# Kernel tuning notes

Hardware: AMD Instinct MI355X
Metric: run time of the kernel (lower is better)

## Reference

```python
import jax, jax.numpy as jnp
import numpy as np

CAPACITY = 8_388_608  # 2**23, power of two -> leftmost_leaf == capacity
N_UPDATES = 1_048_576  # 2**20


def setup_inputs() -> dict:
    key = jax.random.key(0)
    k1, k2, k3 = jax.random.split(key, 3)
    # Existing tree buffer; values[1] is root, values[CAPACITY:2*CAPACITY] are leaves.
    tree_values = jax.random.uniform(k1, (2 * CAPACITY,), dtype=jnp.float32)
    # Distinct leaf indices in [0, CAPACITY): torch scatter-assign with duplicate
    # indices is nondeterministic, so the meaningful case is distinct indices.
    indices = jax.random.permutation(k2, CAPACITY)[:N_UPDATES].astype(jnp.int32)
    values = jax.random.uniform(k3, (N_UPDATES,), dtype=jnp.float32)
    return {"tree_values": tree_values, "indices": indices, "values": values}


def reference(tree_values, indices, values):
    """SegmentTree.__setitem__ with op=add: set leaves, propagate sums to root.

    Returns the updated (2*capacity,) tree buffer.
    """
    capacity = tree_values.shape[0] // 2  # static python int
    depth = int(capacity).bit_length() - 1  # log2(capacity) levels to the root
    # _index_to_leaf: with power-of-two capacity, leaf = idx + capacity (no wrap).
    leaf = indices.astype(jnp.int32) + capacity
    tree = tree_values.at[leaf].set(values)
    idx = leaf
    # Original does torch.unique(idx//2) per level purely as an optimization;
    # duplicate parents recompute the identical value, so plain scatter-set of
    # op(left_child, right_child) is the same math and jit-friendly.
    for _ in range(depth):
        idx = idx // 2
        parent = tree[2 * idx] + tree[2 * idx + 1]
        tree = tree.at[idx].set(parent)
    return tree
```

## Files before the change

kernel.cpp:

```cpp
#include <hip/hip_runtime.h>


typedef unsigned int uint;
typedef unsigned char uchar;

#define NB_COARSE 256
#define CCAP 4608
#define FCAP 512
#define NPB 4096

__global__ void clear_kernel(uint* __restrict__ gcursor) {
    gcursor[threadIdx.x] = threadIdx.x * CCAP;
}

__global__ __launch_bounds__(256)
void coarse_bin_kernel(const int* __restrict__ idx,
                       const float* __restrict__ val,
                       uint* __restrict__ gcursor,
                       uint2* __restrict__ coarse) {
    __shared__ uint hist[NB_COARSE], rbase[NB_COARSE], cur[NB_COARSE];
    const int tid = threadIdx.x;
    hist[tid] = 0u;
    __syncthreads();

    const int i0 = blockIdx.x * NPB;
    uint j[16]; float v[16];
    #pragma unroll
    for (int e = 0; e < 16; ++e) {
        int i = i0 + e * 256 + tid;
        j[e] = (uint)idx[i];
        v[e] = val[i];
        atomicAdd(&hist[j[e] >> 15], 1u);
    }
    __syncthreads();
    rbase[tid] = hist[tid] ? atomicAdd(&gcursor[tid], hist[tid]) : 0u;
    cur[tid] = 0u;
    __syncthreads();
    #pragma unroll
    for (int e = 0; e < 16; ++e) {
        uint cb = j[e] >> 15;
        uint pos = rbase[cb] + atomicAdd(&cur[cb], 1u);
        if (pos < (cb + 1u) * CCAP)
            coarse[pos] = make_uint2(j[e], __float_as_uint(v[e]));
    }
}

__global__ __launch_bounds__(256)
void fine_bin_kernel(const uint* __restrict__ gcursor,
                     const uint2* __restrict__ coarse,
                     uint* __restrict__ fcnt,
                     uint2* __restrict__ fbins) {
    __shared__ uint fcur[16];
    const int b = blockIdx.x, tid = threadIdx.x;
    if (tid < 16) fcur[tid] = 0u;
    __syncthreads();
    uint nb = gcursor[b] - (uint)b * CCAP;
    if (nb > CCAP) nb = CCAP;
    const uint2* my = coarse + (size_t)b * CCAP;
    for (uint k = tid; k < nb; k += 256u) {
        uint2 e = my[k];
        uint fb = (e.x >> 11) & 15u;
        uint r = atomicAdd(&fcur[fb], 1u);
        if (r < FCAP)
            fbins[(((size_t)b * 16u + fb) << 9) + r] = e;
    }
    __syncthreads();
    if (tid < 16) {
        uint c = fcur[tid];
        fcnt[b * 16 + tid] = c > FCAP ? FCAP : c;
    }
}

__global__ __launch_bounds__(256)
void merge_kernel(const float* __restrict__ tree,
                  const uint* __restrict__ fcnt,
                  const uint2* __restrict__ fbins,
                  uchar* __restrict__ l11flag,
                  float* __restrict__ out, int C) {
    __shared__ float slv[2048];
    __shared__ uchar sfl[2048];
    __shared__ float sv[256];
    __shared__ uint  sd[256];

    const int b   = blockIdx.x;
    const int tid = threadIdx.x;

    ((uint2*)sfl)[tid] = make_uint2(0u, 0u);
    __syncthreads();
    uint c = fcnt[b];
    const uint2* mybin = fbins + ((size_t)b << 9);
    for (uint k = tid; k < c; k += 256u) {
        uint2 e = mybin[k];
        uint off = e.x & 2047u;
        slv[off] = __uint_as_float(e.y);
        sfl[off] = 1;
    }
    __syncthreads();

    const int leaf0  = tid * 8;
    const int gleaf0 = b * 2048 + leaf0;

    uint2 fw = *(const uint2*)&sfl[leaf0];
    float4 la = *(const float4*)&slv[leaf0];
    float4 lb = *(const float4*)&slv[leaf0 + 4];
    float4 ta = *(const float4*)(tree + C + gleaf0);
    float4 tb = *(const float4*)(tree + C + gleaf0 + 4);

    float l0 = (fw.x & 0x000000FFu) ? la.x : ta.x;
    float l1 = (fw.x & 0x0000FF00u) ? la.y : ta.y;
    float l2 = (fw.x & 0x00FF0000u) ? la.z : ta.z;
    float l3 = (fw.x & 0xFF000000u) ? la.w : ta.w;
    float l4 = (fw.y & 0x000000FFu) ? lb.x : tb.x;
    float l5 = (fw.y & 0x0000FF00u) ? lb.y : tb.y;
    float l6 = (fw.y & 0x00FF0000u) ? lb.z : tb.z;
    float l7 = (fw.y & 0xFF000000u) ? lb.w : tb.w;

    *(float4*)(out + C + gleaf0)     = make_float4(l0, l1, l2, l3);
    *(float4*)(out + C + gleaf0 + 4) = make_float4(l4, l5, l6, l7);

    uint d10 = (fw.x & 0x0000FFFFu) != 0u;
    uint d11 = (fw.x & 0xFFFF0000u) != 0u;
    uint d12 = (fw.y & 0x0000FFFFu) != 0u;
    uint d13 = (fw.y & 0xFFFF0000u) != 0u;
    float4 t1 = *(const float4*)(tree + (C >> 1) + (gleaf0 >> 1));
    float4 v1;
    v1.x = d10 ? l0 + l1 : t1.x;
    v1.y = d11 ? l2 + l3 : t1.y;
    v1.z = d12 ? l4 + l5 : t1.z;
    v1.w = d13 ? l6 + l7 : t1.w;
    *(float4*)(out + (C >> 1) + (gleaf0 >> 1)) = v1;

    float2 t2 = *(const float2*)(tree + (C >> 2) + (gleaf0 >> 2));
    uint d20 = d10 | d11, d21 = d12 | d13;
    float2 v2;
    v2.x = d20 ? v1.x + v1.y : t2.x;
    v2.y = d21 ? v1.z + v1.w : t2.y;
    *(float2*)(out + (C >> 2) + (gleaf0 >> 2)) = v2;

    float t3 = tree[(C >> 3) + (gleaf0 >> 3)];
    uint d3 = d20 | d21;
    float v3 = d3 ? v2.x + v2.y : t3;
    out[(C >> 3) + (gleaf0 >> 3)] = v3;

    float curv = v3;
    uint  curd = d3;
    const int nb = b * 2048;
    for (int lvl = 4; lvl <= 11; ++lvl) {
        sv[tid] = curv;
        sd[tid] = curd;
        __syncthreads();
        const int A = 2048 >> lvl;
        float nv = 0.f;
        uint  nd = 0u;
        if (tid < A) {
            nd = sd[2 * tid] | sd[2 * tid + 1];
            int node = (C >> lvl) + (nb >> lvl) + tid;
            float tv = tree[node];
            nv = nd ? sv[2 * tid] + sv[2 * tid + 1] : tv;
            out[node] = nv;
        }
        __syncthreads();
        curv = nv;
        curd = nd;
    }
    if (tid == 0) l11flag[b] = (uchar)curd;
}

__global__ __launch_bounds__(1024)
void tail_kernel(const float* __restrict__ tree,
                 const uchar* __restrict__ l11flag,
                 float* __restrict__ out) {
    __shared__ float va[2048];
    __shared__ uint  da[2048];
    const int tid = threadIdx.x;
    for (int i = tid; i < 2048; i += 1024) {
        int p = 2048 + i;
        uint nd = (uint)l11flag[2 * i] | (uint)l11flag[2 * i + 1];
        float v = nd ? out[2 * p] + out[2 * p + 1] : tree[p];
        out[p] = v;
        va[i] = v;
        da[i] = nd;
    }
    __syncthreads();
    for (int M = 1024; M >= 1; M >>= 1) {
        float v = 0.f;
        uint  nd = 0u;
        if (tid < M) {
            int p = M + tid;
            nd = da[2 * tid] | da[2 * tid + 1];
            v = nd ? va[2 * tid] + va[2 * tid + 1] : tree[p];
            out[p] = v;
        }
        __syncthreads();
        if (tid < M) { va[tid] = v; da[tid] = nd; }
        __syncthreads();
    }
    if (tid == 0) out[0] = tree[0];
}

extern "C" void kernel_launch(void* const* d_in, const int* in_sizes, int n_in,
                              void* d_out, int out_size, void* d_ws, size_t ws_size,
                              hipStream_t stream) {
    const float* tree    = (const float*)d_in[0];
    const int*   indices = (const int*)d_in[1];
    const float* values  = (const float*)d_in[2];
    float* out = (float*)d_out;

    const int two_cap = in_sizes[0];
    const int C       = two_cap >> 1;

    uchar* ws = (uchar*)d_ws;
    uint*  gcursor = (uint*)ws;
    uint*  fcnt    = (uint*)(ws + 1024);
    uchar* l11     = ws + 17408;
    uint2* coarse  = (uint2*)(ws + 32768);
    uint2* fbins   = (uint2*)(ws + 32768 + (size_t)NB_COARSE * CCAP * 8);

    clear_kernel<<<1, NB_COARSE, 0, stream>>>(gcursor);

    coarse_bin_kernel<<<NB_COARSE, 256, 0, stream>>>(indices, values,
                                                     gcursor, coarse);

    fine_bin_kernel<<<NB_COARSE, 256, 0, stream>>>(gcursor, coarse,
                                                   fcnt, fbins);

    merge_kernel<<<C / 2048, 256, 0, stream>>>(tree, fcnt, fbins, l11, out, C);

    tail_kernel<<<1, 1024, 0, stream>>>(tree, l11, out);
}
```

Before: 160.5 us.

## Replace shared-memory tree reduction with wavefront shuffles and ballot-mask compaction

The upper-level reductions in the merge and tail kernels move from shared memory plus __syncthreads per level to in-wavefront __shfl pairs. Dirty flags are carried in a 64-bit ballot mask that is compacted with bit-pair ORs at each level. Only one block barrier remains, followed by a small serial finish of levels 10-11, or a single-wave finish in the tail. This is meant to remove the repeated barrier and LDS round-trip overhead in the latency-bound upper levels, at the cost of more ALU work and a serial tid==0 tail.

New measurement: 157.9 us. No clear change (-1.7%).

```diff
diff --git a/kernel.cpp b/kernel.cpp
--- a/kernel.cpp
+++ b/kernel.cpp
@@ -3,11 +3,22 @@
 
 typedef unsigned int uint;
 typedef unsigned char uchar;
+typedef unsigned long long ull;
 
 #define NB_COARSE 256
 #define CCAP 4608
 #define FCAP 512
 #define NPB 4096
+
+__device__ __forceinline__ ull pc64(ull c) {
+    ull x = (c | (c >> 1)) & 0x5555555555555555ull;
+    x = (x | (x >> 1))  & 0x3333333333333333ull;
+    x = (x | (x >> 2))  & 0x0F0F0F0F0F0F0F0Full;
+    x = (x | (x >> 4))  & 0x00FF00FF00FF00FFull;
+    x = (x | (x >> 8))  & 0x0000FFFF0000FFFFull;
+    x = (x | (x >> 16)) & 0x00000000FFFFFFFFull;
+    return x;
+}
 
 __global__ void clear_kernel(uint* __restrict__ gcursor) {
     gcursor[threadIdx.x] = threadIdx.x * CCAP;
@@ -79,11 +90,13 @@
                   float* __restrict__ out, int C) {
     __shared__ float slv[2048];
     __shared__ uchar sfl[2048];
-    __shared__ float sv[256];
-    __shared__ uint  sd[256];
+    __shared__ float swv[4];
+    __shared__ uint  swd[4];
 
     const int b   = blockIdx.x;
     const int tid = threadIdx.x;
+    const int w    = tid >> 6;
+    const int lane = tid & 63;
 
     ((uint2*)sfl)[tid] = make_uint2(0u, 0u);
     __syncthreads();
@@ -139,63 +152,94 @@
 
     float t3 = tree[(C >> 3) + (gleaf0 >> 3)];
     uint d3 = d20 | d21;
-    float v3 = d3 ? v2.x + v2.y : t3;
-    out[(C >> 3) + (gleaf0 >> 3)] = v3;
-
-    float curv = v3;
-    uint  curd = d3;
-    const int nb = b * 2048;
-    for (int lvl = 4; lvl <= 11; ++lvl) {
-        sv[tid] = curv;
-        sd[tid] = curd;
-        __syncthreads();
-        const int A = 2048 >> lvl;
-        float nv = 0.f;
-        uint  nd = 0u;
-        if (tid < A) {
-            nd = sd[2 * tid] | sd[2 * tid + 1];
-            int node = (C >> lvl) + (nb >> lvl) + tid;
-            float tv = tree[node];
-            nv = nd ? sv[2 * tid] + sv[2 * tid + 1] : tv;
-            out[node] = nv;
+    float v = d3 ? v2.x + v2.y : t3;
+    out[(C >> 3) + (gleaf0 >> 3)] = v;
+
+    ull m = __ballot(d3 != 0u);
+    #pragma unroll
+    for (int lvl = 4; lvl <= 9; ++lvl) {
+        float a  = __shfl(v, 2 * lane, 64);
+        float bb = __shfl(v, 2 * lane + 1, 64);
+        m = pc64(m);
+        int n = 64 >> (lvl - 3);
+        if (lane < n) {
+            int node = (C >> lvl) + ((b * 2048 + w * 512) >> lvl) + lane;
+            uint d = (uint)(m >> lane) & 1u;
+            v = d ? a + bb : tree[node];
+            out[node] = v;
         }
-        __syncthreads();
-        curv = nv;
-        curd = nd;
-    }
-    if (tid == 0) l11flag[b] = (uchar)curd;
+    }
+
+    if (lane == 0) { swv[w] = v; swd[w] = (uint)(m & 1ull); }
+    __syncthreads();
+    if (tid == 0) {
+        uint da0 = swd[0] | swd[1], da1 = swd[2] | swd[3];
+        int n10 = (C >> 10) + 2 * b;
+        float v100 = da0 ? swv[0] + swv[1] : tree[n10];
+        float v101 = da1 ? swv[2] + swv[3] : tree[n10 + 1];
+        out[n10]     = v100;
+        out[n10 + 1] = v101;
+        uint d11f = da0 | da1;
+        int n11 = (C >> 11) + b;
+        out[n11] = d11f ? v100 + v101 : tree[n11];
+        l11flag[b] = (uchar)d11f;
+    }
 }
 
 __global__ __launch_bounds__(1024)
 void tail_kernel(const float* __restrict__ tree,
                  const uchar* __restrict__ l11flag,
                  float* __restrict__ out) {
-    __shared__ float va[2048];
-    __shared__ uint  da[2048];
-    const int tid = threadIdx.x;
-    for (int i = tid; i < 2048; i += 1024) {
-        int p = 2048 + i;
-        uint nd = (uint)l11flag[2 * i] | (uint)l11flag[2 * i + 1];
-        float v = nd ? out[2 * p] + out[2 * p + 1] : tree[p];
-        out[p] = v;
-        va[i] = v;
-        da[i] = nd;
-    }
-    __syncthreads();
-    for (int M = 1024; M >= 1; M >>= 1) {
-        float v = 0.f;
-        uint  nd = 0u;
-        if (tid < M) {
-            int p = M + tid;
-            nd = da[2 * tid] | da[2 * tid + 1];
-            v = nd ? va[2 * tid] + va[2 * tid + 1] : tree[p];
-            out[p] = v;
+    __shared__ float s16[16];
+    __shared__ uint  sd16[16];
+    const int t = threadIdx.x, w = t >> 6, lane = t & 63;
+
+    float4 ch = *(const float4*)(out + 4096 + 4 * t);
+    uint fl = ((const uint*)l11flag)[t];
+    uint d0 = (fl & 0x0000FFFFu) != 0u;
+    uint d1 = (fl & 0xFFFF0000u) != 0u;
+    float2 t12 = *(const float2*)(tree + 2048 + 2 * t);
+    float v0 = d0 ? ch.x + ch.y : t12.x;
+    float v1 = d1 ? ch.z + ch.w : t12.y;
+    *(float2*)(out + 2048 + 2 * t) = make_float2(v0, v1);
+    uint d = d0 | d1;
+    float v = d ? v0 + v1 : tree[1024 + t];
+    out[1024 + t] = v;
+
+    ull m = __ballot(d != 0u);
+    #pragma unroll
+    for (int M = 512; M >= 16; M >>= 1) {
+        float a  = __shfl(v, 2 * lane, 64);
+        float bb = __shfl(v, 2 * lane + 1, 64);
+        m = pc64(m);
+        int nw = M >> 4;
+        if (lane < nw) {
+            int node = M + nw * w + lane;
+            uint dd = (uint)(m >> lane) & 1u;
+            v = dd ? a + bb : tree[node];
+            out[node] = v;
         }
-        __syncthreads();
-        if (tid < M) { va[tid] = v; da[tid] = nd; }
-        __syncthreads();
-    }
-    if (tid == 0) out[0] = tree[0];
+    }
+    if (lane == 0) { s16[w] = v; sd16[w] = (uint)(m & 1ull); }
+    __syncthreads();
+
+    if (w == 0) {
+        float vv = lane < 16 ? s16[lane] : 0.f;
+        uint dd  = lane < 16 ? sd16[lane] : 0u;
+        ull mm = __ballot(dd != 0u);
+        #pragma unroll
+        for (int M = 8; M >= 1; M >>= 1) {
+            float a  = __shfl(vv, 2 * lane, 64);
+            float bb = __shfl(vv, 2 * lane + 1, 64);
+            mm = pc64(mm);
+            if (lane < M) {
+                uint d2 = (uint)(mm >> lane) & 1u;
+                vv = d2 ? a + bb : tree[M + lane];
+                out[M + lane] = vv;
+            }
+        }
+        if (lane == 0) out[0] = tree[0];
+    }
 }
 
 extern "C" void kernel_launch(void* const* d_in, const int* in_sizes, int n_in,
@@ -217,14 +261,10 @@
     uint2* fbins   = (uint2*)(ws + 32768 + (size_t)NB_COARSE * CCAP * 8);
 
     clear_kernel<<<1, NB_COARSE, 0, stream>>>(gcursor);
-
     coarse_bin_kernel<<<NB_COARSE, 256, 0, stream>>>(indices, values,
                                                      gcursor, coarse);
-
     fine_bin_kernel<<<NB_COARSE, 256, 0, stream>>>(gcursor, coarse,
                                                    fcnt, fbins);
-
     merge_kernel<<<C / 2048, 256, 0, stream>>>(tree, fcnt, fbins, l11, out, C);
-
     tail_kernel<<<1, 1024, 0, stream>>>(tree, l11, out);
 }
```
